# Kernel optimization log

Hardware: AMD Instinct MI355X
Metric: run time of the kernel (lower is better)

The kernel has to match this reference:

```python
import jax, jax.numpy as jnp
import numpy as np

B, S, D = 16, 1024, 768
H = 12
DH = D // H  # 64

def setup_inputs() -> dict:
    key = jax.random.key(0)
    ks = jax.random.split(key, 7)
    scale = 1.0 / np.sqrt(D)
    return {
        "hidden_states": jax.random.normal(ks[0], (B, S, D), dtype=jnp.float32),
        "Wq": jax.random.normal(ks[1], (D, D), dtype=jnp.float32) * scale,
        "bq": jnp.zeros((D,), dtype=jnp.float32),
        "Wk": jax.random.normal(ks[2], (D, D), dtype=jnp.float32) * scale,
        "bk": jnp.zeros((D,), dtype=jnp.float32),
        "Wv": jax.random.normal(ks[3], (D, D), dtype=jnp.float32) * scale,
        "bv": jnp.zeros((D,), dtype=jnp.float32),
    }

def reference(hidden_states, Wq, bq, Wk, bk, Wv, bv):
    # QKV projections: [B,S,D] -> [B,S,H,DH] -> [B,H,S,DH]
    def proj(W, b):
        y = hidden_states @ W.T + b
        return y.reshape(B, S, H, DH).transpose(0, 2, 1, 3)
    q = proj(Wq, bq)
    k = proj(Wk, bk)
    v = proj(Wv, bv)
    # attention scores [B,H,S,S], scaled by sqrt(d_head)
    scores = jnp.einsum('bhqd,bhkd->bhqk', q, k) / jnp.sqrt(jnp.float32(DH))
    probs = jax.nn.softmax(scores, axis=-1)
    # dropout prob = 0.0 (eval) -> identity
    ctx = jnp.einsum('bhqk,bhkd->bhqd', probs, v)
    ctx = ctx.transpose(0, 2, 1, 3).reshape(B, S, D)
    return ctx
```

## Files before the change

### kernel.cpp

```cpp
#include <hip/hip_runtime.h>
#include <hip/hip_bf16.h>

typedef __attribute__((ext_vector_type(8))) short short8;
typedef __attribute__((ext_vector_type(4))) float float4v;
typedef __attribute__((ext_vector_type(2))) unsigned int uint2v;

#define MFMA_BF16 __builtin_amdgcn_mfma_f32_16x16x32_bf16

__device__ __forceinline__ unsigned short f2b(float f) {
  union { float f; unsigned u; } v; v.f = f;
  unsigned r = v.u + 0x7FFFu + ((v.u >> 16) & 1u);
  return (unsigned short)(r >> 16);
}

__device__ __forceinline__ unsigned pk2(float x, float y) {
  float2 v; v.x = x; v.y = y;
  __hip_bfloat162 h = __float22bfloat162_rn(v);
  union { __hip_bfloat162 h; unsigned u; } c; c.h = h;
  return c.u;
}

__device__ __forceinline__ void gld16(const unsigned short* g, unsigned short* l) {
  __builtin_amdgcn_global_load_lds(
      (const __attribute__((address_space(1))) unsigned int*)g,
      (__attribute__((address_space(3))) unsigned int*)l, 16, 0, 0);
}

__device__ __forceinline__ int swa(int r, int k) {
  return (r << 6) + ((((k >> 3) ^ r ^ (r >> 3)) & 7) << 3) + (k & 7);
}

__global__ __launch_bounds__(256) void cast_all(
    const float* __restrict__ hs, const float* __restrict__ Wq,
    const float* __restrict__ Wk, const float* __restrict__ Wv,
    unsigned short* __restrict__ Xb, unsigned short* __restrict__ Wb) {
  const int blk = blockIdx.x;
  const float* src;
  unsigned short* dst;
  int i;
  if (blk < 12288) {
    i = blk * 256 + threadIdx.x;
    src = hs;
    dst = Xb;
  } else {
    const int x = blk - 12288;
    const int z = x / 576;
    i = (x - z * 576) * 256 + threadIdx.x;
    src = (z == 0) ? Wq : (z == 1 ? Wk : Wv);
    dst = Wb + (size_t)z * 589824;
  }
  float4 f = ((const float4*)src)[i];
  uint2 o;
  o.x = pk2(f.x, f.y);
  o.y = pk2(f.z, f.w);
  ((uint2*)dst)[i] = o;
}

__global__ __launch_bounds__(512) void qkv_gemm(
    const unsigned short* __restrict__ X, const unsigned short* __restrict__ Wall,
    const float* __restrict__ b0, const float* __restrict__ b1, const float* __restrict__ b2,
    unsigned short* __restrict__ O0, unsigned short* __restrict__ O1, unsigned short* __restrict__ OVT) {
  extern __shared__ __align__(16) unsigned short LDS[];

  const int g = blockIdx.x;
  const int orig = (g & 7) * 144 + (g >> 3);
  const int mblk = orig / 18;
  const int nblk = orig - mblk * 18;
  const int m0 = mblk * 256, n0p = nblk * 128;

  const int t = threadIdx.x, w = t >> 6, l = t & 63, qd = l >> 4, col = l & 15;
  const int wm64 = (w & 3) * 64, wn64 = (w >> 2) * 64;
  const int qd8 = qd * 8;

  const int cA0 = t, cA1 = 512 + t, cA2 = 1024 + t, cA3 = 1536 + t;
  const int rA0 = cA0 >> 3, rA1 = cA1 >> 3, rA2 = cA2 >> 3, rA3 = cA3 >> 3;
  const int pA0 = (cA0 ^ rA0 ^ (rA0 >> 3)) & 7, pA1 = (cA1 ^ rA1 ^ (rA1 >> 3)) & 7;
  const int pA2 = (cA2 ^ rA2 ^ (rA2 >> 3)) & 7, pA3 = (cA3 ^ rA3 ^ (rA3 >> 3)) & 7;
  const int cB0 = t, cB1 = 512 + t;
  const int rB0 = cB0 >> 3, rB1 = cB1 >> 3;
  const int pB0 = (cB0 ^ rB0 ^ (rB0 >> 3)) & 7, pB1 = (cB1 ^ rB1 ^ (rB1 >> 3)) & 7;

  const unsigned short* Xa0 = X + (size_t)(m0 + rA0) * 768 + pA0 * 8;
  const unsigned short* Xa1 = X + (size_t)(m0 + rA1) * 768 + pA1 * 8;
  const unsigned short* Xa2 = X + (size_t)(m0 + rA2) * 768 + pA2 * 8;
  const unsigned short* Xa3 = X + (size_t)(m0 + rA3) * 768 + pA3 * 8;
  const unsigned short* Wb0 = Wall + (size_t)(n0p + rB0) * 768 + pB0 * 8;
  const unsigned short* Wb1 = Wall + (size_t)(n0p + rB1) * 768 + pB1 * 8;
  const int dA0 = cA0 * 8, dA1 = cA1 * 8, dA2 = cA2 * 8, dA3 = cA3 * 8;
  const int dB0 = cB0 * 8, dB1 = cB1 * 8;

#define STAGE(kt, sb)                                         \
  do {                                                        \
    unsigned short* SA_ = LDS + (sb)*24576;                   \
    unsigned short* SB_ = SA_ + 16384;                        \
    const int kk_ = (kt)*64;                                  \
    gld16(Xa0 + kk_, SA_ + dA0);                              \
    gld16(Xa1 + kk_, SA_ + dA1);                              \
    gld16(Xa2 + kk_, SA_ + dA2);                              \
    gld16(Xa3 + kk_, SA_ + dA3);                              \
    gld16(Wb0 + kk_, SB_ + dB0);                              \
    gld16(Wb1 + kk_, SB_ + dB1);                              \
  } while (0)

  float4v acc[4][4];
#pragma unroll
  for (int i = 0; i < 4; ++i)
#pragma unroll
    for (int j = 0; j < 4; ++j) acc[i][j] = (float4v)0.0f;

#define COMPUTE(cur)                                                          \
  do {                                                                        \
    const unsigned short* Ar_ = LDS + (cur)*24576;                            \
    const unsigned short* Br_ = Ar_ + 16384;                                  \
    _Pragma("unroll") for (int ks = 0; ks < 2; ++ks) {                        \
      short8 af[4], bf[4];                                                    \
      _Pragma("unroll") for (int mi = 0; mi < 4; ++mi)                        \
          af[mi] = *(const short8*)&Ar_[swa(wm64 + mi * 16 + col,             \
                                            ks * 32 + qd8)];                  \
      _Pragma("unroll") for (int ni = 0; ni < 4; ++ni)                        \
          bf[ni] = *(const short8*)&Br_[swa(wn64 + ni * 16 + col,             \
                                            ks * 32 + qd8)];                  \
      __builtin_amdgcn_s_setprio(1);                                          \
      _Pragma("unroll") for (int mi = 0; mi < 4; ++mi)                        \
          _Pragma("unroll") for (int ni = 0; ni < 4; ++ni)                    \
          acc[mi][ni] = MFMA_BF16(af[mi], bf[ni], acc[mi][ni], 0, 0, 0);      \
      __builtin_amdgcn_s_setprio(0);                                          \
    }                                                                         \
  } while (0)

  STAGE(0, 0);
  STAGE(1, 1);
  asm volatile("s_waitcnt vmcnt(6)" ::: "memory");
  __builtin_amdgcn_s_barrier();
  __builtin_amdgcn_sched_barrier(0);

  int cur = 0;
#pragma unroll 1
  for (int kt = 0; kt < 10; ++kt) {
    const int sb = (cur == 0) ? 2 : cur - 1;
    STAGE(kt + 2, sb);
    COMPUTE(cur);
    asm volatile("s_waitcnt vmcnt(6)" ::: "memory");
    __builtin_amdgcn_s_barrier();
    __builtin_amdgcn_sched_barrier(0);
    cur = (cur == 2) ? 0 : cur + 1;
  }
  COMPUTE(cur);
  asm volatile("s_waitcnt vmcnt(0)" ::: "memory");
  __builtin_amdgcn_s_barrier();
  __builtin_amdgcn_sched_barrier(0);
  cur = (cur == 2) ? 0 : cur + 1;
  COMPUTE(cur);

  const int zz = n0p / 768;
  const int nbase = n0p - zz * 768;

  if (zz < 2) {
    unsigned short* O = (zz == 0) ? O0 : O1;
    const float* bias = (zz == 0) ? b0 : b1;
    const float osc = (zz == 0) ? 0.18033688f : 1.0f;
#pragma unroll
    for (int ni = 0; ni < 4; ++ni) {
      const int n = nbase + wn64 + ni * 16 + col;
      const float bb = bias[n];
#pragma unroll
      for (int mi = 0; mi < 4; ++mi)
#pragma unroll
        for (int r = 0; r < 4; ++r) {
          const int m = m0 + wm64 + mi * 16 + qd * 4 + r;
          O[(size_t)m * 768 + n] = f2b((acc[mi][ni][r] + bb) * osc);
        }
    }
  } else {
    __syncthreads();
    unsigned short* T = LDS;
#pragma unroll
    for (int ni = 0; ni < 4; ++ni) {
      const int nl = wn64 + ni * 16 + col;
      const float bb = b2[nbase + nl];
#pragma unroll
      for (int mi = 0; mi < 4; ++mi) {
        const int ml = wm64 + mi * 16 + qd * 4;
        const int mc = ml >> 3;
        ushort4 o;
        o.x = f2b(acc[mi][ni][0] + bb);
        o.y = f2b(acc[mi][ni][1] + bb);
        o.z = f2b(acc[mi][ni][2] + bb);
        o.w = f2b(acc[mi][ni][3] + bb);
        *(ushort4*)&T[(nl << 8) + (((mc ^ (nl & 31)) & 31) << 3) + (ml & 7)] = o;
      }
    }
    __syncthreads();
    const int nl2 = t >> 2;
    const int seg = t & 3;
    const int nglob = nbase + nl2;
    const int hh = nglob >> 6, dd = nglob & 63;
    const int bb2 = m0 >> 10;
    unsigned short* dstp =
        &OVT[(((size_t)bb2 * 12 + hh) * 64 + dd) * 1024 + (m0 & 1023) + seg * 64];
#pragma unroll
    for (int j = 0; j < 8; ++j) {
      const int mc = seg * 8 + j;
      uint4 vv = *(const uint4*)&T[(nl2 << 8) + (((mc ^ (nl2 & 31)) & 31) << 3)];
      *(uint4*)&dstp[j * 8] = vv;
    }
  }
#undef STAGE
#undef COMPUTE
}

__global__ __launch_bounds__(256) void attn(
    const unsigned short* __restrict__ Q, const unsigned short* __restrict__ K,
    const unsigned short* __restrict__ VT, float* __restrict__ O) {
  __shared__ __align__(16) unsigned short Ks0[4096];
  __shared__ __align__(16) unsigned short Ks1[4096];
  __shared__ __align__(16) unsigned short Vt0[4096];
  __shared__ __align__(16) unsigned short Vt1[4096];

  const int g = blockIdx.x;
  const int orig = (g & 7) * 192 + (g >> 3);
  const int qt = orig & 7;
  const int hb = orig >> 3;
  const int b = hb / 12;
  const int h = hb - b * 12;

  const int t = threadIdx.x, w = t >> 6, l = t & 63, qd = l >> 4, col = l & 15;
  const size_t bh = (size_t)b * 786432 + (size_t)h * 64;
  const unsigned short* Kb = K + bh;
  const unsigned short* VTb = VT + ((size_t)(b * 12 + h)) * 65536;

  short8 qf[2][2];
  {
    const unsigned short* Qg = Q + bh + (size_t)(qt * 128 + w * 32) * 768;
#pragma unroll
    for (int mi = 0; mi < 2; ++mi)
#pragma unroll
      for (int ks = 0; ks < 2; ++ks)
        qf[mi][ks] =
            *(const short8*)&Qg[(size_t)(mi * 16 + col) * 768 + ks * 32 + qd * 8];
  }

  const int c0 = t, c1 = 256 + t;
  const int r0 = c0 >> 3, cc0 = (c0 ^ r0 ^ (r0 >> 3)) & 7;
  const int r1 = c1 >> 3, cc1 = (c1 ^ r1 ^ (r1 >> 3)) & 7;

#define STAGE_K(ktile, dst)                                             \
  do {                                                                  \
    const unsigned short* Kg_ = Kb + (size_t)(ktile)*49152;             \
    gld16(&Kg_[(size_t)r0 * 768 + cc0 * 8], &dst[c0 * 8]);              \
    gld16(&Kg_[(size_t)r1 * 768 + cc1 * 8], &dst[c1 * 8]);              \
  } while (0)

#define STAGE_V(ktile, dst)                                             \
  do {                                                                  \
    const unsigned short* Vg_ = VTb + (ktile)*64;                       \
    gld16(&Vg_[(size_t)r0 * 1024 + cc0 * 8], &dst[c0 * 8]);             \
    gld16(&Vg_[(size_t)r1 * 1024 + cc1 * 8], &dst[c1 * 8]);             \
  } while (0)

  STAGE_K(0, Ks0);
  STAGE_V(0, Vt0);

  float4v acc[2][4];
  float4v accl[2];
#pragma unroll
  for (int mi = 0; mi < 2; ++mi) {
    accl[mi] = (float4v)0.0f;
#pragma unroll
    for (int dt = 0; dt < 4; ++dt) acc[mi][dt] = (float4v)0.0f;
  }

  short8 ones;
#pragma unroll
  for (int j = 0; j < 8; ++j) ones[j] = (short)0x3F80;

  __syncthreads();

#define ATTN_ITER(kt, KsR, VtR, KsW, VtW)                                 \
  do {                                                                    \
    if ((kt) < 15) {                                                      \
      STAGE_K((kt) + 1, KsW);                                             \
      STAGE_V((kt) + 1, VtW);                                             \
    }                                                                     \
    short8 kf[2][4];                                                      \
    _Pragma("unroll") for (int ks = 0; ks < 2; ++ks)                      \
        _Pragma("unroll") for (int ni = 0; ni < 4; ++ni)                  \
        kf[ks][ni] =                                                      \
        *(const short8*)&KsR[swa(ni * 16 + col, ks * 32 + qd * 8)];       \
    float4v sT[2][4];                                                     \
    _Pragma("unroll") for (int mi = 0; mi < 2; ++mi)                      \
        _Pragma("unroll") for (int ni = 0; ni < 4; ++ni)                  \
        sT[mi][ni] = (float4v)0.0f;                                       \
    _Pragma("unroll") for (int ks = 0; ks < 2; ++ks)                      \
        _Pragma("unroll") for (int ni = 0; ni < 4; ++ni) {                \
      sT[0][ni] = MFMA_BF16(kf[ks][ni], qf[0][ks], sT[0][ni], 0, 0, 0);   \
      sT[1][ni] = MFMA_BF16(kf[ks][ni], qf[1][ks], sT[1][ni], 0, 0, 0);   \
    }                                                                     \
    _Pragma("unroll") for (int s = 0; s < 2; ++s) {                       \
      short8 pf[2];                                                       \
      _Pragma("unroll") for (int mi = 0; mi < 2; ++mi) {                  \
        float4v sa = sT[mi][s * 2 + 0];                                   \
        float4v sb = sT[mi][s * 2 + 1];                                   \
        unsigned A0 = pk2(__builtin_amdgcn_exp2f(sa[0]),                  \
                          __builtin_amdgcn_exp2f(sa[1]));                 \
        unsigned A1 = pk2(__builtin_amdgcn_exp2f(sa[2]),                  \
                          __builtin_amdgcn_exp2f(sa[3]));                 \
        unsigned B0 = pk2(__builtin_amdgcn_exp2f(sb[0]),                  \
                          __builtin_amdgcn_exp2f(sb[1]));                 \
        unsigned B1 = pk2(__builtin_amdgcn_exp2f(sb[2]),                  \
                          __builtin_amdgcn_exp2f(sb[3]));                 \
        uint2v x0 = __builtin_amdgcn_permlane32_swap(A0, B0, false, false);   \
        uint2v x1 = __builtin_amdgcn_permlane32_swap(A1, B1, false, false);   \
        uint2v y02 = __builtin_amdgcn_permlane16_swap(x0[0], x0[1], false, false); \
        uint2v y13 = __builtin_amdgcn_permlane16_swap(x1[0], x1[1], false, false); \
        union { unsigned u[4]; short8 v; } pu;                            \
        pu.u[0] = y02[0]; pu.u[1] = y13[0];                               \
        pu.u[2] = y02[1]; pu.u[3] = y13[1];                               \
        pf[mi] = pu.v;                                                    \
      }                                                                   \
      const int kk = s * 32 + qd * 8;                                     \
      _Pragma("unroll") for (int dt = 0; dt < 4; ++dt) {                  \
        short8 vf = *(const short8*)&VtR[swa(dt * 16 + col, kk)];         \
        acc[0][dt] = MFMA_BF16(vf, pf[0], acc[0][dt], 0, 0, 0);           \
        acc[1][dt] = MFMA_BF16(vf, pf[1], acc[1][dt], 0, 0, 0);           \
      }                                                                   \
      accl[0] = MFMA_BF16(ones, pf[0], accl[0], 0, 0, 0);                 \
      accl[1] = MFMA_BF16(ones, pf[1], accl[1], 0, 0, 0);                 \
    }                                                                     \
    __syncthreads();                                                      \
  } while (0)

  for (int kt2 = 0; kt2 < 16; kt2 += 2) {
    ATTN_ITER(kt2, Ks0, Vt0, Ks1, Vt1);
    ATTN_ITER(kt2 + 1, Ks1, Vt1, Ks0, Vt0);
  }

  float* Og = O + (size_t)(b * 1024 + qt * 128) * 768 + h * 64;
#pragma unroll
  for (int mi = 0; mi < 2; ++mi) {
    const float rl = 1.0f / accl[mi][0];
    const int q = w * 32 + mi * 16 + col;
#pragma unroll
    for (int dt = 0; dt < 4; ++dt) {
      float4 o;
      o.x = acc[mi][dt][0] * rl;
      o.y = acc[mi][dt][1] * rl;
      o.z = acc[mi][dt][2] * rl;
      o.w = acc[mi][dt][3] * rl;
      *(float4*)&Og[(size_t)q * 768 + dt * 16 + qd * 4] = o;
    }
  }
#undef STAGE_K
#undef STAGE_V
#undef ATTN_ITER
}

extern "C" void kernel_launch(void* const* d_in, const int* in_sizes, int n_in,
                              void* d_out, int out_size, void* d_ws, size_t ws_size,
                              hipStream_t stream) {
  const float* hs = (const float*)d_in[0];
  const float* Wq = (const float*)d_in[1];
  const float* bq = (const float*)d_in[2];
  const float* Wk = (const float*)d_in[3];
  const float* bk = (const float*)d_in[4];
  const float* Wv = (const float*)d_in[5];
  const float* bv = (const float*)d_in[6];
  float* out = (float*)d_out;
  char* ws = (char*)d_ws;

  unsigned short* Xb = (unsigned short*)ws;
  unsigned short* Wb = (unsigned short*)(ws + 25165824);
  unsigned short* Qb = (unsigned short*)(ws + 28704768);
  unsigned short* Kb = (unsigned short*)(ws + 53870592);
  unsigned short* Vb = (unsigned short*)(ws + 79036416);

  static bool attr_set = false;
  if (!attr_set) {
    hipFuncSetAttribute((const void*)qkv_gemm,
                        hipFuncAttributeMaxDynamicSharedMemorySize, 147456);
    attr_set = true;
  }

  cast_all<<<14016, 256, 0, stream>>>(hs, Wq, Wk, Wv, Xb, Wb);

  qkv_gemm<<<dim3(1152), 512, 147456, stream>>>(Xb, Wb, bq, bk, bv, Qb, Kb, Vb);

  attn<<<dim3(1536), 256, 0, stream>>>(Qb, Kb, Vb, out);
}
```

Baseline: 259.7 us.

## Enlarge QKV GEMM tile to 256x256 with double buffering; add setprio in attention

The QKV projection GEMM now uses 256x256 output tiles instead of 256x128, so each of 8 waves computes a 128x64 sub-tile, and the grid halves to 576 blocks. The pipeline goes from triple to double buffering with a full vmcnt(0) wait each iteration, which lowers LDS use to 128KB. The V-transpose epilogue is adapted to the wider tile. The attention kernel also gains s_setprio around its MFMA blocks. The larger tile raises arithmetic intensity but doubles accumulator registers. The shallower prefetch with full waits, plus fewer blocks on the machine, may expose more memory latency.

```diff
diff --git a/kernel.cpp b/kernel.cpp
--- a/kernel.cpp
+++ b/kernel.cpp
@@ -56,72 +56,66 @@
   ((uint2*)dst)[i] = o;
 }
 
-__global__ __launch_bounds__(512) void qkv_gemm(
+__global__ __launch_bounds__(512, 2) void qkv_gemm(
     const unsigned short* __restrict__ X, const unsigned short* __restrict__ Wall,
     const float* __restrict__ b0, const float* __restrict__ b1, const float* __restrict__ b2,
     unsigned short* __restrict__ O0, unsigned short* __restrict__ O1, unsigned short* __restrict__ OVT) {
   extern __shared__ __align__(16) unsigned short LDS[];
 
   const int g = blockIdx.x;
-  const int orig = (g & 7) * 144 + (g >> 3);
-  const int mblk = orig / 18;
-  const int nblk = orig - mblk * 18;
-  const int m0 = mblk * 256, n0p = nblk * 128;
+  const int orig = (g & 7) * 72 + (g >> 3);
+  const int mblk = orig / 9;
+  const int nblk = orig - mblk * 9;
+  const int m0 = mblk * 256, n0p = nblk * 256;
 
   const int t = threadIdx.x, w = t >> 6, l = t & 63, qd = l >> 4, col = l & 15;
-  const int wm64 = (w & 3) * 64, wn64 = (w >> 2) * 64;
+  const int wm = (w >> 2) * 128, wn = (w & 3) * 64;
   const int qd8 = qd * 8;
 
-  const int cA0 = t, cA1 = 512 + t, cA2 = 1024 + t, cA3 = 1536 + t;
-  const int rA0 = cA0 >> 3, rA1 = cA1 >> 3, rA2 = cA2 >> 3, rA3 = cA3 >> 3;
-  const int pA0 = (cA0 ^ rA0 ^ (rA0 >> 3)) & 7, pA1 = (cA1 ^ rA1 ^ (rA1 >> 3)) & 7;
-  const int pA2 = (cA2 ^ rA2 ^ (rA2 >> 3)) & 7, pA3 = (cA3 ^ rA3 ^ (rA3 >> 3)) & 7;
-  const int cB0 = t, cB1 = 512 + t;
-  const int rB0 = cB0 >> 3, rB1 = cB1 >> 3;
-  const int pB0 = (cB0 ^ rB0 ^ (rB0 >> 3)) & 7, pB1 = (cB1 ^ rB1 ^ (rB1 >> 3)) & 7;
-
-  const unsigned short* Xa0 = X + (size_t)(m0 + rA0) * 768 + pA0 * 8;
-  const unsigned short* Xa1 = X + (size_t)(m0 + rA1) * 768 + pA1 * 8;
-  const unsigned short* Xa2 = X + (size_t)(m0 + rA2) * 768 + pA2 * 8;
-  const unsigned short* Xa3 = X + (size_t)(m0 + rA3) * 768 + pA3 * 8;
-  const unsigned short* Wb0 = Wall + (size_t)(n0p + rB0) * 768 + pB0 * 8;
-  const unsigned short* Wb1 = Wall + (size_t)(n0p + rB1) * 768 + pB1 * 8;
-  const int dA0 = cA0 * 8, dA1 = cA1 * 8, dA2 = cA2 * 8, dA3 = cA3 * 8;
-  const int dB0 = cB0 * 8, dB1 = cB1 * 8;
-
-#define STAGE(kt, sb)                                         \
-  do {                                                        \
-    unsigned short* SA_ = LDS + (sb)*24576;                   \
-    unsigned short* SB_ = SA_ + 16384;                        \
-    const int kk_ = (kt)*64;                                  \
-    gld16(Xa0 + kk_, SA_ + dA0);                              \
-    gld16(Xa1 + kk_, SA_ + dA1);                              \
-    gld16(Xa2 + kk_, SA_ + dA2);                              \
-    gld16(Xa3 + kk_, SA_ + dA3);                              \
-    gld16(Wb0 + kk_, SB_ + dB0);                              \
-    gld16(Wb1 + kk_, SB_ + dB1);                              \
-  } while (0)
-
-  float4v acc[4][4];
-#pragma unroll
-  for (int i = 0; i < 4; ++i)
+  int rr[4], pp[4];
+#pragma unroll
+  for (int i = 0; i < 4; ++i) {
+    const int c = i * 512 + t;
+    const int r = c >> 3;
+    rr[i] = r;
+    pp[i] = (c ^ r ^ (r >> 3)) & 7;
+  }
+  const unsigned short* Xbase = X + (size_t)m0 * 768;
+  const unsigned short* Wbase = Wall + (size_t)n0p * 768;
+
+#define STAGE(kt, buf)                                                        \
+  do {                                                                        \
+    unsigned short* SA_ = LDS + (buf)*32768;                                  \
+    unsigned short* SB_ = SA_ + 16384;                                        \
+    const int kk_ = (kt)*64;                                                  \
+    _Pragma("unroll") for (int i = 0; i < 4; ++i)                             \
+        gld16(Xbase + (size_t)rr[i] * 768 + kk_ + pp[i] * 8,                  \
+              SA_ + (i * 512 + t) * 8);                                       \
+    _Pragma("unroll") for (int i = 0; i < 4; ++i)                             \
+        gld16(Wbase + (size_t)rr[i] * 768 + kk_ + pp[i] * 8,                  \
+              SB_ + (i * 512 + t) * 8);                                       \
+  } while (0)
+
+  float4v acc[8][4];
+#pragma unroll
+  for (int i = 0; i < 8; ++i)
 #pragma unroll
     for (int j = 0; j < 4; ++j) acc[i][j] = (float4v)0.0f;
 
-#define COMPUTE(cur)                                                          \
+#define COMPUTE(buf)                                                          \
   do {                                                                        \
-    const unsigned short* Ar_ = LDS + (cur)*24576;                            \
+    const unsigned short* Ar_ = LDS + (buf)*32768;                            \
     const unsigned short* Br_ = Ar_ + 16384;                                  \
     _Pragma("unroll") for (int ks = 0; ks < 2; ++ks) {                        \
-      short8 af[4], bf[4];                                                    \
-      _Pragma("unroll") for (int mi = 0; mi < 4; ++mi)                        \
-          af[mi] = *(const short8*)&Ar_[swa(wm64 + mi * 16 + col,             \
+      short8 af[8], bf[4];                                                    \
+      _Pragma("unroll") for (int mi = 0; mi < 8; ++mi)                        \
+          af[mi] = *(const short8*)&Ar_[swa(wm + mi * 16 + col,               \
                                             ks * 32 + qd8)];                  \
       _Pragma("unroll") for (int ni = 0; ni < 4; ++ni)                        \
-          bf[ni] = *(const short8*)&Br_[swa(wn64 + ni * 16 + col,             \
+          bf[ni] = *(const short8*)&Br_[swa(wn + ni * 16 + col,               \
                                             ks * 32 + qd8)];                  \
       __builtin_amdgcn_s_setprio(1);                                          \
-      _Pragma("unroll") for (int mi = 0; mi < 4; ++mi)                        \
+      _Pragma("unroll") for (int mi = 0; mi < 8; ++mi)                        \
           _Pragma("unroll") for (int ni = 0; ni < 4; ++ni)                    \
           acc[mi][ni] = MFMA_BF16(af[mi], bf[ni], acc[mi][ni], 0, 0, 0);      \
       __builtin_amdgcn_s_setprio(0);                                          \
@@ -129,27 +123,20 @@
   } while (0)
 
   STAGE(0, 0);
-  STAGE(1, 1);
-  asm volatile("s_waitcnt vmcnt(6)" ::: "memory");
-  __builtin_amdgcn_s_barrier();
-  __builtin_amdgcn_sched_barrier(0);
-
-  int cur = 0;
-#pragma unroll 1
-  for (int kt = 0; kt < 10; ++kt) {
-    const int sb = (cur == 0) ? 2 : cur - 1;
-    STAGE(kt + 2, sb);
-    COMPUTE(cur);
-    asm volatile("s_waitcnt vmcnt(6)" ::: "memory");
-    __builtin_amdgcn_s_barrier();
-    __builtin_amdgcn_sched_barrier(0);
-    cur = (cur == 2) ? 0 : cur + 1;
-  }
-  COMPUTE(cur);
   asm volatile("s_waitcnt vmcnt(0)" ::: "memory");
   __builtin_amdgcn_s_barrier();
   __builtin_amdgcn_sched_barrier(0);
-  cur = (cur == 2) ? 0 : cur + 1;
+
+  int cur = 0;
+#pragma unroll 1
+  for (int kt = 0; kt < 11; ++kt) {
+    STAGE(kt + 1, cur ^ 1);
+    COMPUTE(cur);
+    asm volatile("s_waitcnt vmcnt(0)" ::: "memory");
+    __builtin_amdgcn_s_barrier();
+    __builtin_amdgcn_sched_barrier(0);
+    cur ^= 1;
+  }
   COMPUTE(cur);
 
   const int zz = n0p / 768;
@@ -161,13 +148,13 @@
     const float osc = (zz == 0) ? 0.18033688f : 1.0f;
 #pragma unroll
     for (int ni = 0; ni < 4; ++ni) {
-      const int n = nbase + wn64 + ni * 16 + col;
+      const int n = nbase + wn + ni * 16 + col;
       const float bb = bias[n];
 #pragma unroll
-      for (int mi = 0; mi < 4; ++mi)
+      for (int mi = 0; mi < 8; ++mi)
 #pragma unroll
         for (int r = 0; r < 4; ++r) {
-          const int m = m0 + wm64 + mi * 16 + qd * 4 + r;
+          const int m = m0 + wm + mi * 16 + qd * 4 + r;
           O[(size_t)m * 768 + n] = f2b((acc[mi][ni][r] + bb) * osc);
         }
     }
@@ -176,11 +163,11 @@
     unsigned short* T = LDS;
 #pragma unroll
     for (int ni = 0; ni < 4; ++ni) {
-      const int nl = wn64 + ni * 16 + col;
+      const int nl = wn + ni * 16 + col;
       const float bb = b2[nbase + nl];
 #pragma unroll
-      for (int mi = 0; mi < 4; ++mi) {
-        const int ml = wm64 + mi * 16 + qd * 4;
+      for (int mi = 0; mi < 8; ++mi) {
+        const int ml = wm + mi * 16 + qd * 4;
         const int mc = ml >> 3;
         ushort4 o;
         o.x = f2b(acc[mi][ni][0] + bb);
@@ -191,16 +178,16 @@
       }
     }
     __syncthreads();
-    const int nl2 = t >> 2;
-    const int seg = t & 3;
+    const int nl2 = t >> 1;
+    const int seg = t & 1;
     const int nglob = nbase + nl2;
     const int hh = nglob >> 6, dd = nglob & 63;
     const int bb2 = m0 >> 10;
     unsigned short* dstp =
-        &OVT[(((size_t)bb2 * 12 + hh) * 64 + dd) * 1024 + (m0 & 1023) + seg * 64];
-#pragma unroll
-    for (int j = 0; j < 8; ++j) {
-      const int mc = seg * 8 + j;
+        &OVT[(((size_t)bb2 * 12 + hh) * 64 + dd) * 1024 + (m0 & 1023) + seg * 128];
+#pragma unroll
+    for (int j = 0; j < 16; ++j) {
+      const int mc = seg * 16 + j;
       uint4 vv = *(const uint4*)&T[(nl2 << 8) + (((mc ^ (nl2 & 31)) & 31) << 3)];
       *(uint4*)&dstp[j * 8] = vv;
     }
@@ -291,11 +278,13 @@
     _Pragma("unroll") for (int mi = 0; mi < 2; ++mi)                      \
         _Pragma("unroll") for (int ni = 0; ni < 4; ++ni)                  \
         sT[mi][ni] = (float4v)0.0f;                                       \
+    __builtin_amdgcn_s_setprio(1);                                        \
     _Pragma("unroll") for (int ks = 0; ks < 2; ++ks)                      \
         _Pragma("unroll") for (int ni = 0; ni < 4; ++ni) {                \
       sT[0][ni] = MFMA_BF16(kf[ks][ni], qf[0][ks], sT[0][ni], 0, 0, 0);   \
       sT[1][ni] = MFMA_BF16(kf[ks][ni], qf[1][ks], sT[1][ni], 0, 0, 0);   \
     }                                                                     \
+    __builtin_amdgcn_s_setprio(0);                                        \
     _Pragma("unroll") for (int s = 0; s < 2; ++s) {                       \
       short8 pf[2];                                                       \
       _Pragma("unroll") for (int mi = 0; mi < 2; ++mi) {                  \
@@ -319,6 +308,7 @@
         pf[mi] = pu.v;                                                    \
       }                                                                   \
       const int kk = s * 32 + qd * 8;                                     \
+      __builtin_amdgcn_s_setprio(1);                                      \
       _Pragma("unroll") for (int dt = 0; dt < 4; ++dt) {                  \
         short8 vf = *(const short8*)&VtR[swa(dt * 16 + col, kk)];         \
         acc[0][dt] = MFMA_BF16(vf, pf[0], acc[0][dt], 0, 0, 0);           \
@@ -326,6 +316,7 @@
       }                                                                   \
       accl[0] = MFMA_BF16(ones, pf[0], accl[0], 0, 0, 0);                 \
       accl[1] = MFMA_BF16(ones, pf[1], accl[1], 0, 0, 0);                 \
+      __builtin_amdgcn_s_setprio(0);                                      \
     }                                                                     \
     __syncthreads();                                                      \
   } while (0)
@@ -377,13 +368,13 @@
   static bool attr_set = false;
   if (!attr_set) {
     hipFuncSetAttribute((const void*)qkv_gemm,
-                        hipFuncAttributeMaxDynamicSharedMemorySize, 147456);
+                        hipFuncAttributeMaxDynamicSharedMemorySize, 131072);
     attr_set = true;
   }
 
   cast_all<<<14016, 256, 0, stream>>>(hs, Wq, Wk, Wv, Xb, Wb);
 
-  qkv_gemm<<<dim3(1152), 512, 147456, stream>>>(Xb, Wb, bq, bk, bv, Qb, Kb, Vb);
+  qkv_gemm<<<dim3(576), 512, 131072, stream>>>(Xb, Wb, bq, bk, bv, Qb, Kb, Vb);
 
   attn<<<dim3(1536), 256, 0, stream>>>(Qb, Kb, Vb, out);
 }
```

After: 257.9 us. No clear change (-0.7%).

## Load V fragments directly from global to registers and add MFMA priority hints

Applied to the files above, without the earlier changes.

The transposed V tile is no longer staged through double-buffered LDS. Each lane now loads its V fragments straight from global memory into registers at the start of each key tile, which halves LDS usage and removes the LDS reads for V. s_setprio is also raised around the MFMA blocks so matrix work gets issue priority over other waves. The trade-off is that V loads are exposed global latency within the same iteration, and nothing is prefetched a tile ahead.

```diff
diff --git a/kernel.cpp b/kernel.cpp
--- a/kernel.cpp
+++ b/kernel.cpp
@@ -214,8 +214,6 @@
     const unsigned short* __restrict__ VT, float* __restrict__ O) {
   __shared__ __align__(16) unsigned short Ks0[4096];
   __shared__ __align__(16) unsigned short Ks1[4096];
-  __shared__ __align__(16) unsigned short Vt0[4096];
-  __shared__ __align__(16) unsigned short Vt1[4096];
 
   const int g = blockIdx.x;
   const int orig = (g & 7) * 192 + (g >> 3);
@@ -251,15 +249,7 @@
     gld16(&Kg_[(size_t)r1 * 768 + cc1 * 8], &dst[c1 * 8]);              \
   } while (0)
 
-#define STAGE_V(ktile, dst)                                             \
-  do {                                                                  \
-    const unsigned short* Vg_ = VTb + (ktile)*64;                       \
-    gld16(&Vg_[(size_t)r0 * 1024 + cc0 * 8], &dst[c0 * 8]);             \
-    gld16(&Vg_[(size_t)r1 * 1024 + cc1 * 8], &dst[c1 * 8]);             \
-  } while (0)
-
   STAGE_K(0, Ks0);
-  STAGE_V(0, Vt0);
 
   float4v acc[2][4];
   float4v accl[2];
@@ -274,14 +264,18 @@
 #pragma unroll
   for (int j = 0; j < 8; ++j) ones[j] = (short)0x3F80;
 
+  const unsigned short* Vl = VTb + (size_t)col * 1024 + qd * 8;
+
   __syncthreads();
 
-#define ATTN_ITER(kt, KsR, VtR, KsW, VtW)                                 \
+#define ATTN_ITER(kt, KsR, KsW)                                           \
   do {                                                                    \
-    if ((kt) < 15) {                                                      \
-      STAGE_K((kt) + 1, KsW);                                             \
-      STAGE_V((kt) + 1, VtW);                                             \
-    }                                                                     \
+    short8 vf[2][4];                                                      \
+    _Pragma("unroll") for (int s = 0; s < 2; ++s)                         \
+        _Pragma("unroll") for (int dt = 0; dt < 4; ++dt)                  \
+        vf[s][dt] = *(const short8*)&Vl[(size_t)dt * 16384 +              \
+                                        (kt)*64 + s * 32];                \
+    if ((kt) < 15) STAGE_K((kt) + 1, KsW);                                \
     short8 kf[2][4];                                                      \
     _Pragma("unroll") for (int ks = 0; ks < 2; ++ks)                      \
         _Pragma("unroll") for (int ni = 0; ni < 4; ++ni)                  \
@@ -291,11 +285,13 @@
     _Pragma("unroll") for (int mi = 0; mi < 2; ++mi)                      \
         _Pragma("unroll") for (int ni = 0; ni < 4; ++ni)                  \
         sT[mi][ni] = (float4v)0.0f;                                       \
+    __builtin_amdgcn_s_setprio(1);                                        \
     _Pragma("unroll") for (int ks = 0; ks < 2; ++ks)                      \
         _Pragma("unroll") for (int ni = 0; ni < 4; ++ni) {                \
       sT[0][ni] = MFMA_BF16(kf[ks][ni], qf[0][ks], sT[0][ni], 0, 0, 0);   \
       sT[1][ni] = MFMA_BF16(kf[ks][ni], qf[1][ks], sT[1][ni], 0, 0, 0);   \
     }                                                                     \
+    __builtin_amdgcn_s_setprio(0);                                        \
     _Pragma("unroll") for (int s = 0; s < 2; ++s) {                       \
       short8 pf[2];                                                       \
       _Pragma("unroll") for (int mi = 0; mi < 2; ++mi) {                  \
@@ -318,21 +314,21 @@
         pu.u[2] = y02[1]; pu.u[3] = y13[1];                               \
         pf[mi] = pu.v;                                                    \
       }                                                                   \
-      const int kk = s * 32 + qd * 8;                                     \
+      __builtin_amdgcn_s_setprio(1);                                      \
       _Pragma("unroll") for (int dt = 0; dt < 4; ++dt) {                  \
-        short8 vf = *(const short8*)&VtR[swa(dt * 16 + col, kk)];         \
-        acc[0][dt] = MFMA_BF16(vf, pf[0], acc[0][dt], 0, 0, 0);           \
-        acc[1][dt] = MFMA_BF16(vf, pf[1], acc[1][dt], 0, 0, 0);           \
+        acc[0][dt] = MFMA_BF16(vf[s][dt], pf[0], acc[0][dt], 0, 0, 0);    \
+        acc[1][dt] = MFMA_BF16(vf[s][dt], pf[1], acc[1][dt], 0, 0, 0);    \
       }                                                                   \
       accl[0] = MFMA_BF16(ones, pf[0], accl[0], 0, 0, 0);                 \
       accl[1] = MFMA_BF16(ones, pf[1], accl[1], 0, 0, 0);                 \
+      __builtin_amdgcn_s_setprio(0);                                      \
     }                                                                     \
     __syncthreads();                                                      \
   } while (0)
 
   for (int kt2 = 0; kt2 < 16; kt2 += 2) {
-    ATTN_ITER(kt2, Ks0, Vt0, Ks1, Vt1);
-    ATTN_ITER(kt2 + 1, Ks1, Vt1, Ks0, Vt0);
+    ATTN_ITER(kt2, Ks0, Ks1);
+    ATTN_ITER(kt2 + 1, Ks1, Ks0);
   }
 
   float* Og = O + (size_t)(b * 1024 + qt * 128) * 768 + h * 64;
@@ -351,7 +347,6 @@
     }
   }
 #undef STAGE_K
-#undef STAGE_V
 #undef ATTN_ITER
 }
 
```

New measurement: 285.9 us. 1.1x slower.
